# Kernel tuning notes

Hardware: AMD Instinct MI355X
Metric: run time of the kernel (lower is better)

The kernel has to match this reference:

```python
import jax, jax.numpy as jnp
import numpy as np

B = 512        # batch
TW = 45        # raw wav token length
C = 512        # n_embd
H = 8          # heads
L = 8          # decoder layers
V = 1000       # wav vocab
NLAB = 5       # label vocab
HID = 2048     # 4*C mlp hidden
OH = 768       # output head hidden
WIN, TRAIN = 30, 44
LN_EPS = 1e-5


def _build_mask(t):
    # triangular (strict upper) + sliding-window lower band, tiled 3x3 over segments
    m = np.triu(np.ones((TRAIN, TRAIN), dtype=bool), 1)
    for i in range(WIN, TRAIN):
        m[i, : i - WIN + 1] = True
    m = m[:t, :t]
    return jnp.asarray(np.tile(m, (3, 3)))  # [3t, 3t], True = masked


def setup_inputs() -> dict:
    key = jax.random.key(0)
    ks = iter(jax.random.split(key, 64))

    def rn(shape, s=0.02):
        return jax.random.normal(next(ks), shape, jnp.float32) * s

    inp = {
        'label': jax.random.randint(next(ks), (B, 1), 0, NLAB),
        'wav1': jax.random.randint(next(ks), (B, TW), 0, V),
        'wav2': jax.random.randint(next(ks), (B, TW), 0, V),
        # embeddings
        'emb_label': rn((NLAB, C), 1.0),
        'emb_w1': rn((V, C), 1.0),
        'emb_w2': rn((V, C), 1.0),
        # per-layer stacked params (leading dim L) for lax.scan
        'ln1_g': jnp.ones((L, 3, C), jnp.float32),
        'ln1_b': jnp.zeros((L, 3, C), jnp.float32),
        'ln2_g': jnp.ones((L, 3, C), jnp.float32),
        'ln2_b': jnp.zeros((L, 3, C), jnp.float32),
        'Wq': rn((L, C, C)), 'bq': jnp.zeros((L, C), jnp.float32),
        'Wk': rn((L, C, C)), 'bk': jnp.zeros((L, C), jnp.float32),
        'Wv': rn((L, C, C)), 'bv': jnp.zeros((L, C), jnp.float32),
        'Wp': rn((L, C, C)), 'bp': jnp.zeros((L, C), jnp.float32),
        'W1': rn((L, C, HID)), 'b1': jnp.zeros((L, HID), jnp.float32),
        'W2': rn((L, HID, C)), 'b2': jnp.zeros((L, C), jnp.float32),
        # output heads
        'o1W1': rn((C, OH)), 'o1b1': jnp.zeros((OH,), jnp.float32),
        'o1W2': rn((OH, V)), 'o1b2': jnp.zeros((V,), jnp.float32),
        'o2W1': rn((C, OH)), 'o2b1': jnp.zeros((OH,), jnp.float32),
        'o2W2': rn((OH, V)), 'o2b2': jnp.zeros((V,), jnp.float32),
    }
    return inp


def _forward(label, wav1, wav2, emb_label, emb_w1, emb_w2,
             ln1_g, ln1_b, ln2_g, ln2_b, Wq, bq, Wk, bk, Wv, bv, Wp, bp,
             W1, b1, W2, b2, o1W1, o1b1, o1W2, o1b2, o2W1, o2b1, o2W2, o2b2):
    wav1_src, wav1_tgt = wav1[:, :-1], wav1[:, 1:]
    wav2_src, wav2_tgt = wav2[:, :-1], wav2[:, 1:]
    b, t = wav1_src.shape
    label_rep = jnp.broadcast_to(label, (b, t))

    feat = jnp.concatenate([emb_label[label_rep], emb_w1[wav1_src], emb_w2[wav2_src]], axis=1)  # [B,3t,C]
    mask = _build_mask(t)  # [3t,3t] bool
    hd = C // H

    def ln3(x, g, be):
        # three separate LayerNorms over the 3 equal segments
        xr = x.reshape(b, 3, t, C)
        mu = xr.mean(-1, keepdims=True)
        var = xr.var(-1, keepdims=True)
        xn = (xr - mu) * jax.lax.rsqrt(var + LN_EPS)
        return (xn * g[None, :, None, :] + be[None, :, None, :]).reshape(b, 3 * t, C)

    def layer(x, p):
        g1, be1, g2, be2, wq, bq_, wk, bk_, wv, bv_, wp, bp_, w1, b1_, w2, b2_ = p
        h = ln3(x, g1, be1)
        q = (h @ wq + bq_).reshape(b, 3 * t, H, hd).transpose(0, 2, 1, 3)
        k = (h @ wk + bk_).reshape(b, 3 * t, H, hd).transpose(0, 2, 1, 3)
        v = (h @ wv + bv_).reshape(b, 3 * t, H, hd).transpose(0, 2, 1, 3)
        att = jnp.einsum('bhqd,bhkd->bhqk', q, k) * (1.0 / np.sqrt(hd))
        att = jnp.where(mask[None, None], -jnp.inf, att)
        att = jax.nn.softmax(att, axis=-1)
        y = jnp.einsum('bhqk,bhkd->bhqd', att, v).transpose(0, 2, 1, 3).reshape(b, 3 * t, C)
        x = x + (y @ wp + bp_)
        h2 = ln3(x, g2, be2)
        m = jax.nn.gelu(h2 @ w1 + b1_, approximate=False) @ w2 + b2_
        return x + m, None

    params = (ln1_g, ln1_b, ln2_g, ln2_b, Wq, bq, Wk, bk, Wv, bv, Wp, bp, W1, b1, W2, b2)
    x, _ = jax.lax.scan(layer, feat, params)

    wav1_pred = (x[:, t:2 * t] @ o1W1 + o1b1) @ o1W2 + o1b2  # [B,t,V]
    wav2_pred = (x[:, 2 * t:] @ o2W1 + o2b1) @ o2W2 + o2b2

    def ce(logits, tgt):
        lp = jax.nn.log_softmax(logits.reshape(-1, V).astype(jnp.float32), axis=-1)
        return -jnp.mean(jnp.take_along_axis(lp, tgt.reshape(-1, 1), axis=1))

    return ce(wav1_pred, wav1_tgt) + ce(wav2_pred, wav2_tgt)


def reference(label, wav1, wav2, emb_label, emb_w1, emb_w2,
              ln1_g, ln1_b, ln2_g, ln2_b, Wq, bq, Wk, bk, Wv, bv, Wp, bp,
              W1, b1, W2, b2, o1W1, o1b1, o1W2, o1b2, o2W1, o2b1, o2W2, o2b2):
    return _forward(label, wav1, wav2, emb_label, emb_w1, emb_w2,
                    ln1_g, ln1_b, ln2_g, ln2_b, Wq, bq, Wk, bk, Wv, bv, Wp, bp,
                    W1, b1, W2, b2, o1W1, o1b1, o1W2, o1b2, o2W1, o2b1, o2W2, o2b2)
```

## Files before the change

kernel.cpp:

```cpp
#include <hip/hip_runtime.h>

typedef __attribute__((ext_vector_type(4))) float f32x4;
typedef __attribute__((ext_vector_type(8))) __bf16 bf16x8;
typedef __attribute__((ext_vector_type(4))) __bf16 bf16x4;
typedef __attribute__((ext_vector_type(2))) __bf16 bf16x2;
typedef __attribute__((ext_vector_type(8))) unsigned short u16x8;

#define NB 512
#define TT 44
#define S3 132
#define CC 512
#define NH 8
#define NL 8
#define NV 1000
#define VP 1024
#define HID 2048
#define OH 768
#define WINW 30
#define QKVN 1536

#define HROWS (NB*TT)

#define WT_OFF   0ull
#define WC1T_OFF 50331648ull
#define WC2T_OFF 51380224ull
#define BC1_OFF  52428800ull
#define BC2_OFF  52432896ull
#define BQKV_OFF 52436992ull
#define LOSS_OFF 52486144ull
#define FIXED_SZ 52666368ull
#define PER_CHB  811008ull

#define LAYER_WELEMS 3145728ull

__device__ inline bf16x8 zero8() { u16x8 z = (u16x8)0; return *(bf16x8*)&z; }

#define STAGE(bufi, ktile) do { \
  _Pragma("unroll") \
  for (int i_ = 0; i_ < 2; ++i_) { \
    int off_ = wid * 2048 + i_ * 1024; \
    int myoff_ = off_ + lane * 16; \
    int row_ = myoff_ >> 6; \
    int colb_ = (myoff_ & 63) ^ ((row_ & 3) << 4); \
    const char* sa_ = (const char*)(A + (arow + row_) * (size_t)KDIM + ((size_t)(ktile) << 5)) + colb_; \
    const char* sb_ = (const char*)(Bt + (brow + row_) * (size_t)KDIM + ((size_t)(ktile) << 5)) + colb_; \
    __builtin_amdgcn_global_load_lds((const __attribute__((address_space(1))) void*)sa_, \
        (__attribute__((address_space(3))) void*)((char*)&As[bufi][0] + off_), 16, 0, 0); \
    __builtin_amdgcn_global_load_lds((const __attribute__((address_space(1))) void*)sb_, \
        (__attribute__((address_space(3))) void*)((char*)&Bs[bufi][0] + off_), 16, 0, 0); \
  } \
} while (0)

#define PHASE(CURB, KTV, MORE) do { \
  bf16x8 af_[4], bfv_[4]; \
  _Pragma("unroll") \
  for (int mi_ = 0; mi_ < 4; ++mi_) \
    af_[mi_] = *(const bf16x8*)&As[CURB][(wr * 64 + mi_ * 16 + l15) * 32 + ((lk ^ swz) * 8)]; \
  _Pragma("unroll") \
  for (int ni_ = 0; ni_ < 4; ++ni_) \
    bfv_[ni_] = *(const bf16x8*)&Bs[CURB][(wc * 64 + ni_ * 16 + l15) * 32 + ((lk ^ swz) * 8)]; \
  if (MORE) STAGE(((CURB) + 2) % 3, (KTV) + 2); \
  _Pragma("unroll") \
  for (int mi_ = 0; mi_ < 4; ++mi_) \
    _Pragma("unroll") \
    for (int ni_ = 0; ni_ < 4; ++ni_) \
      acc[mi_][ni_] = __builtin_amdgcn_mfma_f32_16x16x32_bf16(af_[mi_], bfv_[ni_], acc[mi_][ni_], 0, 0, 0); \
  if (MORE) { asm volatile("s_waitcnt vmcnt(4)\n\ts_barrier" ::: "memory"); } \
  else      { asm volatile("s_waitcnt vmcnt(0)\n\ts_barrier" ::: "memory"); } \
} while (0)

template<int KDIM, int EPI, typename OutT, typename ResT>
__global__ __launch_bounds__(256) void gemm_bt(
    const __bf16* __restrict__ A, const __bf16* __restrict__ Bt,
    const float* __restrict__ bias, const ResT* __restrict__ resid,
    OutT* __restrict__ C, int M, int N)
{
    __shared__ __bf16 As[3][128 * 32];
    __shared__ __bf16 Bs[3][128 * 32];
    const int tid = threadIdx.x, lane = tid & 63, wid = tid >> 6;
    const int l15 = lane & 15, lk = lane >> 4;
    const int wr = wid >> 1, wc = wid & 1;
    const int swz = l15 & 3;

    const int nwg = gridDim.x * gridDim.y;
    const int orig = blockIdx.y * gridDim.x + blockIdx.x;
    const int qq = nwg >> 3, rr = nwg & 7;
    const int xcd = orig & 7, loc = orig >> 3;
    const int wg = (xcd < rr ? xcd * (qq + 1) : rr * (qq + 1) + (xcd - rr) * qq) + loc;
    const int bn = wg % gridDim.x, bm = wg / gridDim.x;

    f32x4 acc[4][4];
#pragma unroll
    for (int i = 0; i < 4; ++i)
#pragma unroll
        for (int j = 0; j < 4; ++j) acc[i][j] = (f32x4)0.f;

    const size_t arow = (size_t)bm * 128;
    const size_t brow = (size_t)bn * 128;
    constexpr int KT = KDIM >> 5;
    constexpr int M3 = (KT - 2) / 3;

    STAGE(0, 0);
    STAGE(1, 1);
    asm volatile("s_waitcnt vmcnt(4)\n\ts_barrier" ::: "memory");

    for (int t3 = 0; t3 < M3; ++t3) {
        const int kt = t3 * 3;
        PHASE(0, kt, true);
        PHASE(1, kt + 1, true);
        PHASE(2, kt + 2, true);
    }
#pragma unroll
    for (int p = 3 * M3; p < KT; ++p) {
        const int pb = p % 3;
        if (pb == 0)      { if (p <= KT - 3) PHASE(0, p, true); else PHASE(0, p, false); }
        else if (pb == 1) { if (p <= KT - 3) PHASE(1, p, true); else PHASE(1, p, false); }
        else              { if (p <= KT - 3) PHASE(2, p, true); else PHASE(2, p, false); }
    }

#pragma unroll
    for (int mi = 0; mi < 4; ++mi) {
#pragma unroll
        for (int ni = 0; ni < 4; ++ni) {
            int n = bn * 128 + wc * 64 + ni * 16 + l15;
            float bv = (EPI & 1) ? bias[n] : 0.f;
#pragma unroll
            for (int r = 0; r < 4; ++r) {
                int m = bm * 128 + wr * 64 + mi * 16 + lk * 4 + r;
                float v = acc[mi][ni][r] + bv;
                if (EPI & 2) v += (float)resid[(size_t)m * N + n];
                if (EPI & 4) v = v / (1.f + __expf(-1.702f * v));
                C[(size_t)m * N + n] = (OutT)v;
            }
        }
    }
}

#define KLS 68
#define VTS 164
__global__ __launch_bounds__(256) void attn_k(const __bf16* __restrict__ QKV,
                                              __bf16* __restrict__ Y)
{
    __shared__ __bf16 Kl[144 * KLS];
    __shared__ __bf16 Ql[144 * KLS];
    __shared__ __bf16 Vt[64 * VTS];
    __shared__ __bf16 Pl[4][16 * VTS];
    const int tid = threadIdx.x, lane = tid & 63, wid = tid >> 6;
    const int l15 = lane & 15, lk = lane >> 4;
    const int bh = blockIdx.x;
    const int b = bh >> 3, h = bh & 7;
    const size_t base = ((size_t)b * S3) * QKVN + h * 64;
    const size_t ybase = ((size_t)b * S3) * CC + h * 64;

    for (int i = tid; i < S3 * 8; i += 256) {
        int s = i >> 3, c = (i & 7) * 8;
        bf16x8 qv = *(const bf16x8*)(QKV + base + (size_t)s * QKVN + c);
        bf16x8 kv = *(const bf16x8*)(QKV + base + (size_t)s * QKVN + 512 + c);
        *(bf16x8*)&Ql[s * KLS + c] = qv;
        *(bf16x8*)&Kl[s * KLS + c] = kv;
    }
    for (int i = tid; i < (S3 / 2) * 8; i += 256) {
        int s2 = i >> 3, d0 = (i & 7) * 8;
        int s = s2 * 2;
        bf16x8 v0 = *(const bf16x8*)(QKV + base + (size_t)s * QKVN + 1024 + d0);
        bf16x8 v1 = *(const bf16x8*)(QKV + base + (size_t)(s + 1) * QKVN + 1024 + d0);
#pragma unroll
        for (int j = 0; j < 8; ++j) {
            bf16x2 pr; pr[0] = v0[j]; pr[1] = v1[j];
            *(bf16x2*)&Vt[(d0 + j) * VTS + s] = pr;
        }
    }
    for (int i = tid; i < 64 * 32; i += 256) {
        int d = i >> 5, s = 132 + (i & 31);
        Vt[d * VTS + s] = (__bf16)0.f;
    }
    for (int i = lane; i < 16 * 20; i += 64) {
        int r = i / 20, c2 = 144 + (i % 20);
        Pl[wid][r * VTS + c2] = (__bf16)0.f;
    }
    __syncthreads();

    for (int qb = wid; qb < 9; qb += 4) {
        int sq = qb * 16 + l15;
        int sqe = sq < S3 ? sq : (S3 - 1);
        bf16x8 qf0 = *(const bf16x8*)&Ql[(qb * 16 + l15) * KLS + 0 * 32 + lk * 8];
        bf16x8 qf1 = *(const bf16x8*)&Ql[(qb * 16 + l15) * KLS + 1 * 32 + lk * 8];
        f32x4 st[9];
#pragma unroll
        for (int kt = 0; kt < 9; ++kt) {
            f32x4 a = (f32x4)0.f;
            bf16x8 kf0 = *(const bf16x8*)&Kl[(kt * 16 + l15) * KLS + 0 * 32 + lk * 8];
            bf16x8 kf1 = *(const bf16x8*)&Kl[(kt * 16 + l15) * KLS + 1 * 32 + lk * 8];
            a = __builtin_amdgcn_mfma_f32_16x16x32_bf16(kf0, qf0, a, 0, 0, 0);
            a = __builtin_amdgcn_mfma_f32_16x16x32_bf16(kf1, qf1, a, 0, 0, 0);
            st[kt] = a;
        }
        int qm = sqe % TT;
        float mx = -1e30f;
#pragma unroll
        for (int kt = 0; kt < 9; ++kt)
#pragma unroll
            for (int r = 0; r < 4; ++r) {
                int sk = kt * 16 + lk * 4 + r;
                float sv = st[kt][r] * 0.125f;
                int kk = sk % TT;
                bool msk = (sk >= S3) || (kk > qm) || (qm >= WINW && kk <= qm - WINW);
                sv = msk ? -INFINITY : sv;
                st[kt][r] = sv;
                mx = fmaxf(mx, sv);
            }
        mx = fmaxf(mx, __shfl_xor(mx, 16));
        mx = fmaxf(mx, __shfl_xor(mx, 32));
        float sum = 0.f;
#pragma unroll
        for (int kt = 0; kt < 9; ++kt)
#pragma unroll
            for (int r = 0; r < 4; ++r) {
                float p = __expf(st[kt][r] - mx);
                st[kt][r] = p;
                sum += p;
            }
        sum += __shfl_xor(sum, 16);
        sum += __shfl_xor(sum, 32);
        float inv = 1.f / sum;
#pragma unroll
        for (int kt = 0; kt < 9; ++kt) {
            bf16x4 pk;
#pragma unroll
            for (int r = 0; r < 4; ++r) pk[r] = (__bf16)(st[kt][r] * inv);
            *(bf16x4*)&Pl[wid][l15 * VTS + kt * 16 + lk * 4] = pk;
        }
#pragma unroll
        for (int dt = 0; dt < 4; ++dt) {
            f32x4 o = (f32x4)0.f;
#pragma unroll
            for (int ks = 0; ks < 5; ++ks) {
                bf16x8 pa = *(const bf16x8*)&Pl[wid][l15 * VTS + ks * 32 + lk * 8];
                bf16x8 vb = *(const bf16x8*)&Vt[(dt * 16 + l15) * VTS + ks * 32 + lk * 8];
                o = __builtin_amdgcn_mfma_f32_16x16x32_bf16(pa, vb, o, 0, 0, 0);
            }
            int d = dt * 16 + l15;
#pragma unroll
            for (int r = 0; r < 4; ++r) {
                int sqr = qb * 16 + lk * 4 + r;
                if (sqr < S3) Y[ybase + (size_t)sqr * CC + d] = (__bf16)o[r];
            }
        }
    }
}

__global__ __launch_bounds__(256) void ln3_k(const __bf16* __restrict__ X,
                                             const float* __restrict__ g,
                                             const float* __restrict__ be,
                                             __bf16* __restrict__ Hb)
{
    int row = blockIdx.x * 4 + (threadIdx.x >> 6);
    int lane = threadIdx.x & 63;
    int seg = (row % S3) / TT;
    bf16x8 xv = *(const bf16x8*)(X + (size_t)row * CC + lane * 8);
    float vv[8];
    float s = 0.f, ss = 0.f;
#pragma unroll
    for (int j = 0; j < 8; ++j) { vv[j] = (float)xv[j]; s += vv[j]; ss += vv[j] * vv[j]; }
#pragma unroll
    for (int o = 32; o; o >>= 1) { s += __shfl_xor(s, o); ss += __shfl_xor(ss, o); }
    float mu = s * (1.f / CC);
    float var = ss * (1.f / CC) - mu * mu;
    float rs = rsqrtf(var + 1e-5f);
    const float* gp = g + seg * CC + lane * 8;
    const float* bp = be + seg * CC + lane * 8;
    __bf16* op = Hb + (size_t)row * CC + lane * 8;
#pragma unroll
    for (int j = 0; j < 8; ++j) op[j] = (__bf16)((vv[j] - mu) * rs * gp[j] + bp[j]);
}

__global__ __launch_bounds__(128) void embed_k(const int* __restrict__ label,
                                               const int* __restrict__ wav1,
                                               const int* __restrict__ wav2,
                                               const float* __restrict__ el,
                                               const float* __restrict__ e1,
                                               const float* __restrict__ e2,
                                               __bf16* __restrict__ X, int b0)
{
    int row = blockIdx.x;
    int b = b0 + row / S3, p = row % S3;
    int seg = p / TT, pos = p % TT;
    int idx; const float* src;
    if (seg == 0) { idx = label[b]; src = el; }
    else if (seg == 1) { idx = wav1[b * 45 + pos]; src = e1; }
    else { idx = wav2[b * 45 + pos]; src = e2; }
    float4 v = *((const float4*)(src + (size_t)idx * CC) + threadIdx.x);
    __bf16* dst = X + (size_t)row * CC + threadIdx.x * 4;
    dst[0] = (__bf16)v.x; dst[1] = (__bf16)v.y; dst[2] = (__bf16)v.z; dst[3] = (__bf16)v.w;
}

__global__ void transpose_cast(const float* __restrict__ in, __bf16* __restrict__ out,
                               int R, int Cin, int Np, long long inStride, long long outStride)
{
    __shared__ float t[32][33];
    in += (size_t)blockIdx.z * inStride;
    out += (size_t)blockIdx.z * outStride;
    int r0 = blockIdx.x * 32, c0 = blockIdx.y * 32;
    int tx = threadIdx.x, ty = threadIdx.y;
#pragma unroll
    for (int k2 = 0; k2 < 4; ++k2) {
        int r = r0 + ty + k2 * 8, c = c0 + tx;
        t[ty + k2 * 8][tx] = (r < R && c < Cin) ? in[(size_t)r * Cin + c] : 0.f;
    }
    __syncthreads();
#pragma unroll
    for (int k2 = 0; k2 < 4; ++k2) {
        int c = c0 + ty + k2 * 8, r = r0 + tx;
        if (c < Np && r < R) out[(size_t)c * R + r] = (__bf16)t[tx][ty + k2 * 8];
    }
}

__global__ void cast_k(const float* __restrict__ in, __bf16* __restrict__ out, int n)
{
    int i = blockIdx.x * 256 + threadIdx.x;
    if (i < n) out[i] = (__bf16)in[i];
}

__global__ void build_bqkv(const float* __restrict__ bq, const float* __restrict__ bk,
                           const float* __restrict__ bv, float* __restrict__ out)
{
    int i = blockIdx.x * 256 + threadIdx.x;
    if (i >= NL * QKVN) return;
    int l = i / QKVN, c = i % QKVN;
    float v = (c < 512) ? bq[l * 512 + c] : (c < 1024 ? bk[l * 512 + c - 512] : bv[l * 512 + c - 1024]);
    out[i] = v;
}

__global__ __launch_bounds__(128) void gather_cast(const __bf16* __restrict__ X,
                                                   __bf16* __restrict__ out, int segoff)
{
    int row = blockIdx.x;
    int b = row / TT, s2 = row % TT;
    const uint2* src = (const uint2*)(X + ((size_t)b * S3 + segoff + s2) * CC) + threadIdx.x;
    uint2* dst = (uint2*)(out + (size_t)row * CC) + threadIdx.x;
    *dst = *src;
}

__global__ __launch_bounds__(256) void combo_bias(const float* __restrict__ b1,
                                                  const float* __restrict__ W2,
                                                  const float* __restrict__ b2,
                                                  float* __restrict__ out)
{
    int v = blockIdx.x;
    if (v >= VP) return;
    float s = 0.f;
    if (v < NV) {
        for (int o = threadIdx.x; o < OH; o += 256) s += b1[o] * W2[o * NV + v];
    }
#pragma unroll
    for (int o = 32; o; o >>= 1) s += __shfl_xor(s, o);
    __shared__ float w4[4];
    if ((threadIdx.x & 63) == 0) w4[threadIdx.x >> 6] = s;
    __syncthreads();
    if (threadIdx.x == 0) out[v] = (v < NV ? b2[v] : 0.f) + w4[0] + w4[1] + w4[2] + w4[3];
}

__global__ __launch_bounds__(256) void ce_k(const float* __restrict__ logits,
                                            const int* __restrict__ wav,
                                            float* __restrict__ loss)
{
    int row = blockIdx.x * 4 + (threadIdx.x >> 6);
    int lane = threadIdx.x & 63;
    const float* lg = logits + (size_t)row * VP;
    int b = row / TT, s2 = row % TT;
    int tgt = wav[b * 45 + s2 + 1];
    float m = -1e30f;
    for (int i = lane; i < NV; i += 64) m = fmaxf(m, lg[i]);
#pragma unroll
    for (int o = 32; o; o >>= 1) m = fmaxf(m, __shfl_xor(m, o));
    float sum = 0.f;
    for (int i = lane; i < NV; i += 64) sum += __expf(lg[i] - m);
#pragma unroll
    for (int o = 32; o; o >>= 1) sum += __shfl_xor(sum, o);
    if (lane == 0) loss[row] = m + logf(sum) - lg[tgt];
}

__global__ __launch_bounds__(256) void ce_sum(const float* __restrict__ loss, float* __restrict__ out)
{
    float s = 0.f;
    for (int i = threadIdx.x; i < 2 * HROWS; i += 256) s += loss[i];
#pragma unroll
    for (int o = 32; o; o >>= 1) s += __shfl_xor(s, o);
    __shared__ float w4[4];
    if ((threadIdx.x & 63) == 0) w4[threadIdx.x >> 6] = s;
    __syncthreads();
    if (threadIdx.x == 0) out[0] = (w4[0] + w4[1] + w4[2] + w4[3]) * (1.f / HROWS);
}

extern "C" void kernel_launch(void* const* d_in, const int* in_sizes, int n_in,
                              void* d_out, int out_size, void* d_ws, size_t ws_size,
                              hipStream_t stream)
{
    int chb;
    if      (ws_size >= FIXED_SZ + 512ull * PER_CHB) chb = 512;
    else if (ws_size >= FIXED_SZ + 256ull * PER_CHB) chb = 256;
    else if (ws_size >= FIXED_SZ + 128ull * PER_CHB) chb = 128;
    else return;
    const int nch = NB / chb;
    const int crows = chb * S3;
    const int chr = chb * TT;

    const int*   label = (const int*)d_in[0];
    const int*   wav1  = (const int*)d_in[1];
    const int*   wav2  = (const int*)d_in[2];
    const float* el    = (const float*)d_in[3];
    const float* e1    = (const float*)d_in[4];
    const float* e2    = (const float*)d_in[5];
    const float* ln1g  = (const float*)d_in[6];
    const float* ln1b  = (const float*)d_in[7];
    const float* ln2g  = (const float*)d_in[8];
    const float* ln2b  = (const float*)d_in[9];
    const float* Wq    = (const float*)d_in[10];
    const float* bq    = (const float*)d_in[11];
    const float* Wk    = (const float*)d_in[12];
    const float* bk    = (const float*)d_in[13];
    const float* Wv    = (const float*)d_in[14];
    const float* bv    = (const float*)d_in[15];
    const float* Wp    = (const float*)d_in[16];
    const float* bp    = (const float*)d_in[17];
    const float* W1    = (const float*)d_in[18];
    const float* b1    = (const float*)d_in[19];
    const float* W2    = (const float*)d_in[20];
    const float* b2    = (const float*)d_in[21];
    const float* o1W1  = (const float*)d_in[22];
    const float* o1b1  = (const float*)d_in[23];
    const float* o1W2  = (const float*)d_in[24];
    const float* o1b2  = (const float*)d_in[25];
    const float* o2W1  = (const float*)d_in[26];
    const float* o2b1  = (const float*)d_in[27];
    const float* o2W2  = (const float*)d_in[28];
    const float* o2b2  = (const float*)d_in[29];

    char* ws = (char*)d_ws;
    __bf16* WT    = (__bf16*)(ws + WT_OFF);
    __bf16* Wc1T  = (__bf16*)(ws + WC1T_OFF);
    __bf16* Wc2T  = (__bf16*)(ws + WC2T_OFF);
    float*  bc1   = (float*)(ws + BC1_OFF);
    float*  bc2   = (float*)(ws + BC2_OFF);
    float*  bqkv  = (float*)(ws + BQKV_OFF);
    float*  lossb = (float*)(ws + LOSS_OFF);
    __bf16* X     = (__bf16*)(ws + FIXED_SZ);
    __bf16* Hb    = (__bf16*)(ws + FIXED_SZ + (size_t)chb * 135168ull);
    char*   AR    = ws + FIXED_SZ + (size_t)chb * 270336ull;
    __bf16* o1W2T = (__bf16*)(AR + 0);
    __bf16* o2W2T = (__bf16*)(AR + 1572864);
    __bf16* o1W1b = (__bf16*)(AR + 3145728);
    __bf16* o2W1b = (__bf16*)(AR + 3932160);
    __bf16* qkvb   = (__bf16*)AR;
    __bf16* yb_    = Hb;
    __bf16* hidden = (__bf16*)AR;
    float*  logits = (float*)AR;
    __bf16* Xseg   = Hb;
    float*  outF   = (float*)d_out;

    dim3 tb(32, 8);
    transpose_cast<<<dim3(16, 16, NL), tb, 0, stream>>>(Wq, WT + 0,       CC, CC, CC, (long long)CC * CC, (long long)LAYER_WELEMS);
    transpose_cast<<<dim3(16, 16, NL), tb, 0, stream>>>(Wk, WT + 262144,  CC, CC, CC, (long long)CC * CC, (long long)LAYER_WELEMS);
    transpose_cast<<<dim3(16, 16, NL), tb, 0, stream>>>(Wv, WT + 524288,  CC, CC, CC, (long long)CC * CC, (long long)LAYER_WELEMS);
    transpose_cast<<<dim3(16, 16, NL), tb, 0, stream>>>(Wp, WT + 786432,  CC, CC, CC, (long long)CC * CC, (long long)LAYER_WELEMS);
    transpose_cast<<<dim3(16, 64, NL), tb, 0, stream>>>(W1, WT + 1048576, CC, HID, HID, (long long)CC * HID, (long long)LAYER_WELEMS);
    transpose_cast<<<dim3(64, 16, NL), tb, 0, stream>>>(W2, WT + 2097152, HID, CC, CC, (long long)HID * CC, (long long)LAYER_WELEMS);
    transpose_cast<<<dim3(24, 32, 1), tb, 0, stream>>>(o1W2, o1W2T, OH, NV, VP, 0, 0);
    transpose_cast<<<dim3(24, 32, 1), tb, 0, stream>>>(o2W2, o2W2T, OH, NV, VP, 0, 0);
    cast_k<<<(CC * OH + 255) / 256, 256, 0, stream>>>(o1W1, o1W1b, CC * OH);
    cast_k<<<(CC * OH + 255) / 256, 256, 0, stream>>>(o2W1, o2W1b, CC * OH);
    gemm_bt<OH, 0, __bf16, float><<<dim3(4, 8), 256, 0, stream>>>(o1W2T, o1W1b, nullptr, nullptr, Wc1T, VP, CC);
    gemm_bt<OH, 0, __bf16, float><<<dim3(4, 8), 256, 0, stream>>>(o2W2T, o2W1b, nullptr, nullptr, Wc2T, VP, CC);
    combo_bias<<<VP, 256, 0, stream>>>(o1b1, o1W2, o1b2, bc1);
    combo_bias<<<VP, 256, 0, stream>>>(o2b1, o2W2, o2b2, bc2);
    build_bqkv<<<(NL * QKVN + 255) / 256, 256, 0, stream>>>(bq, bk, bv, bqkv);

    for (int c = 0; c < nch; ++c) {
        int b0 = c * chb;
        embed_k<<<crows, 128, 0, stream>>>(label, wav1, wav2, el, e1, e2, X, b0);

        for (int l = 0; l < NL; ++l) {
            const __bf16* WqkvT = WT + (size_t)l * LAYER_WELEMS;
            const __bf16* WpT   = WT + (size_t)l * LAYER_WELEMS + 786432;
            const __bf16* W1T   = WT + (size_t)l * LAYER_WELEMS + 1048576;
            const __bf16* W2T   = WT + (size_t)l * LAYER_WELEMS + 2097152;

            ln3_k<<<crows / 4, 256, 0, stream>>>(X, ln1g + l * 3 * CC, ln1b + l * 3 * CC, Hb);
            gemm_bt<CC, 1, __bf16, float><<<dim3(QKVN / 128, crows / 128), 256, 0, stream>>>(Hb, WqkvT, bqkv + l * QKVN, nullptr, qkvb, crows, QKVN);
            attn_k<<<chb * NH, 256, 0, stream>>>(qkvb, yb_);
            gemm_bt<CC, 3, __bf16, __bf16><<<dim3(4, crows / 128), 256, 0, stream>>>(yb_, WpT, bp + l * CC, X, X, crows, CC);
            ln3_k<<<crows / 4, 256, 0, stream>>>(X, ln2g + l * 3 * CC, ln2b + l * 3 * CC, Hb);
            gemm_bt<CC, 5, __bf16, float><<<dim3(16, crows / 128), 256, 0, stream>>>(Hb, W1T, b1 + l * HID, nullptr, hidden, crows, HID);
            gemm_bt<HID, 3, __bf16, __bf16><<<dim3(4, crows / 128), 256, 0, stream>>>(hidden, W2T, b2 + l * CC, X, X, crows, CC);
        }

        gather_cast<<<chr, 128, 0, stream>>>(X, Xseg, TT);
        gemm_bt<CC, 1, float, float><<<dim3(VP / 128, chr / 128), 256, 0, stream>>>(Xseg, Wc1T, bc1, nullptr, logits, chr, VP);
        ce_k<<<chr / 4, 256, 0, stream>>>(logits, wav1 + b0 * 45, lossb + c * chr);
        gather_cast<<<chr, 128, 0, stream>>>(X, Xseg, 2 * TT);
        gemm_bt<CC, 1, float, float><<<dim3(VP / 128, chr / 128), 256, 0, stream>>>(Xseg, Wc2T, bc2, nullptr, logits, chr, VP);
        ce_k<<<chr / 4, 256, 0, stream>>>(logits, wav2 + b0 * 45, lossb + HROWS + c * chr);
    }

    ce_sum<<<1, 256, 0, stream>>>(lossb, outF);
}
```

Before: 7.333 ms.

## Skip fully masked attention tiles, fuse segment gather into head GEMM, bf16 logits

Precomputes a per-lane validity mask in attention and skips QK MFMAs, masking and exp work for 16-key tiles that are fully masked across the wavefront. It removes the gather_cast kernel by adding an EPI flag that remaps A rows to the wav segments inside the GEMM loads. It also writes the output-head logits as bf16 and reads them as bf16 pairs in the cross-entropy kernel, halving logits traffic. Storing logits in bf16 may reduce loss precision, and the divergent tile skipping adds branching.

```diff
diff --git a/kernel.cpp b/kernel.cpp
--- a/kernel.cpp
+++ b/kernel.cpp
@@ -35,6 +35,8 @@
 
 __device__ inline bf16x8 zero8() { u16x8 z = (u16x8)0; return *(bf16x8*)&z; }
 
+#define AROW(hr_) ((EPI & 8) ? (size_t)(((unsigned)(hr_) / 44u) * 132u + (unsigned)segoff + ((unsigned)(hr_) % 44u)) : (size_t)(hr_))
+
 #define STAGE(bufi, ktile) do { \
   _Pragma("unroll") \
   for (int i_ = 0; i_ < 2; ++i_) { \
@@ -42,7 +44,7 @@
     int myoff_ = off_ + lane * 16; \
     int row_ = myoff_ >> 6; \
     int colb_ = (myoff_ & 63) ^ ((row_ & 3) << 4); \
-    const char* sa_ = (const char*)(A + (arow + row_) * (size_t)KDIM + ((size_t)(ktile) << 5)) + colb_; \
+    const char* sa_ = (const char*)(A + AROW(arow + row_) * (size_t)KDIM + ((size_t)(ktile) << 5)) + colb_; \
     const char* sb_ = (const char*)(Bt + (brow + row_) * (size_t)KDIM + ((size_t)(ktile) << 5)) + colb_; \
     __builtin_amdgcn_global_load_lds((const __attribute__((address_space(1))) void*)sa_, \
         (__attribute__((address_space(3))) void*)((char*)&As[bufi][0] + off_), 16, 0, 0); \
@@ -73,7 +75,7 @@
 __global__ __launch_bounds__(256) void gemm_bt(
     const __bf16* __restrict__ A, const __bf16* __restrict__ Bt,
     const float* __restrict__ bias, const ResT* __restrict__ resid,
-    OutT* __restrict__ C, int M, int N)
+    OutT* __restrict__ C, int M, int N, int segoff)
 {
     __shared__ __bf16 As[3][128 * 32];
     __shared__ __bf16 Bs[3][128 * 32];
@@ -183,43 +185,65 @@
     for (int qb = wid; qb < 9; qb += 4) {
         int sq = qb * 16 + l15;
         int sqe = sq < S3 ? sq : (S3 - 1);
+        int qm = sqe % TT;
+        unsigned long long lmask = 0ull;
+#pragma unroll
+        for (int kt = 0; kt < 9; ++kt)
+#pragma unroll
+            for (int r = 0; r < 4; ++r) {
+                int sk = kt * 16 + lk * 4 + r;
+                int kk = sk % TT;
+                bool ok = (sk < S3) && (kk <= qm) && (qm < WINW || kk > qm - WINW);
+                if (ok) lmask |= 1ull << (kt * 4 + r);
+            }
+        unsigned needmask = 0;
+#pragma unroll
+        for (int kt = 0; kt < 9; ++kt)
+            if (__any((int)((lmask >> (kt * 4)) & 15ull))) needmask |= 1u << kt;
+
         bf16x8 qf0 = *(const bf16x8*)&Ql[(qb * 16 + l15) * KLS + 0 * 32 + lk * 8];
         bf16x8 qf1 = *(const bf16x8*)&Ql[(qb * 16 + l15) * KLS + 1 * 32 + lk * 8];
         f32x4 st[9];
 #pragma unroll
         for (int kt = 0; kt < 9; ++kt) {
-            f32x4 a = (f32x4)0.f;
-            bf16x8 kf0 = *(const bf16x8*)&Kl[(kt * 16 + l15) * KLS + 0 * 32 + lk * 8];
-            bf16x8 kf1 = *(const bf16x8*)&Kl[(kt * 16 + l15) * KLS + 1 * 32 + lk * 8];
-            a = __builtin_amdgcn_mfma_f32_16x16x32_bf16(kf0, qf0, a, 0, 0, 0);
-            a = __builtin_amdgcn_mfma_f32_16x16x32_bf16(kf1, qf1, a, 0, 0, 0);
-            st[kt] = a;
-        }
-        int qm = sqe % TT;
+            if (needmask & (1u << kt)) {
+                f32x4 a = (f32x4)0.f;
+                bf16x8 kf0 = *(const bf16x8*)&Kl[(kt * 16 + l15) * KLS + 0 * 32 + lk * 8];
+                bf16x8 kf1 = *(const bf16x8*)&Kl[(kt * 16 + l15) * KLS + 1 * 32 + lk * 8];
+                a = __builtin_amdgcn_mfma_f32_16x16x32_bf16(kf0, qf0, a, 0, 0, 0);
+                a = __builtin_amdgcn_mfma_f32_16x16x32_bf16(kf1, qf1, a, 0, 0, 0);
+                st[kt] = a;
+            }
+        }
         float mx = -1e30f;
 #pragma unroll
-        for (int kt = 0; kt < 9; ++kt)
-#pragma unroll
-            for (int r = 0; r < 4; ++r) {
-                int sk = kt * 16 + lk * 4 + r;
-                float sv = st[kt][r] * 0.125f;
-                int kk = sk % TT;
-                bool msk = (sk >= S3) || (kk > qm) || (qm >= WINW && kk <= qm - WINW);
-                sv = msk ? -INFINITY : sv;
-                st[kt][r] = sv;
-                mx = fmaxf(mx, sv);
-            }
+        for (int kt = 0; kt < 9; ++kt) {
+            if (needmask & (1u << kt)) {
+#pragma unroll
+                for (int r = 0; r < 4; ++r) {
+                    bool ok = (lmask >> (kt * 4 + r)) & 1ull;
+                    float sv = ok ? st[kt][r] * 0.125f : -INFINITY;
+                    st[kt][r] = sv;
+                    mx = fmaxf(mx, sv);
+                }
+            }
+        }
         mx = fmaxf(mx, __shfl_xor(mx, 16));
         mx = fmaxf(mx, __shfl_xor(mx, 32));
         float sum = 0.f;
 #pragma unroll
-        for (int kt = 0; kt < 9; ++kt)
-#pragma unroll
-            for (int r = 0; r < 4; ++r) {
-                float p = __expf(st[kt][r] - mx);
-                st[kt][r] = p;
-                sum += p;
-            }
+        for (int kt = 0; kt < 9; ++kt) {
+            if (needmask & (1u << kt)) {
+#pragma unroll
+                for (int r = 0; r < 4; ++r) {
+                    float p = __expf(st[kt][r] - mx);
+                    st[kt][r] = p;
+                    sum += p;
+                }
+            } else {
+                st[kt] = (f32x4)0.f;
+            }
+        }
         sum += __shfl_xor(sum, 16);
         sum += __shfl_xor(sum, 32);
         float inv = 1.f / sum;
@@ -331,16 +355,6 @@
     out[i] = v;
 }
 
-__global__ __launch_bounds__(128) void gather_cast(const __bf16* __restrict__ X,
-                                                   __bf16* __restrict__ out, int segoff)
-{
-    int row = blockIdx.x;
-    int b = row / TT, s2 = row % TT;
-    const uint2* src = (const uint2*)(X + ((size_t)b * S3 + segoff + s2) * CC) + threadIdx.x;
-    uint2* dst = (uint2*)(out + (size_t)row * CC) + threadIdx.x;
-    *dst = *src;
-}
-
 __global__ __launch_bounds__(256) void combo_bias(const float* __restrict__ b1,
                                                   const float* __restrict__ W2,
                                                   const float* __restrict__ b2,
@@ -360,24 +374,30 @@
     if (threadIdx.x == 0) out[v] = (v < NV ? b2[v] : 0.f) + w4[0] + w4[1] + w4[2] + w4[3];
 }
 
-__global__ __launch_bounds__(256) void ce_k(const float* __restrict__ logits,
+__global__ __launch_bounds__(256) void ce_k(const __bf16* __restrict__ logits,
                                             const int* __restrict__ wav,
                                             float* __restrict__ loss)
 {
     int row = blockIdx.x * 4 + (threadIdx.x >> 6);
     int lane = threadIdx.x & 63;
-    const float* lg = logits + (size_t)row * VP;
+    const __bf16* lg = logits + (size_t)row * VP;
     int b = row / TT, s2 = row % TT;
     int tgt = wav[b * 45 + s2 + 1];
     float m = -1e30f;
-    for (int i = lane; i < NV; i += 64) m = fmaxf(m, lg[i]);
+    for (int i2 = lane; i2 < NV / 2; i2 += 64) {
+        bf16x2 pr = *(const bf16x2*)(lg + 2 * i2);
+        m = fmaxf(m, fmaxf((float)pr[0], (float)pr[1]));
+    }
 #pragma unroll
     for (int o = 32; o; o >>= 1) m = fmaxf(m, __shfl_xor(m, o));
     float sum = 0.f;
-    for (int i = lane; i < NV; i += 64) sum += __expf(lg[i] - m);
+    for (int i2 = lane; i2 < NV / 2; i2 += 64) {
+        bf16x2 pr = *(const bf16x2*)(lg + 2 * i2);
+        sum += __expf((float)pr[0] - m) + __expf((float)pr[1] - m);
+    }
 #pragma unroll
     for (int o = 32; o; o >>= 1) sum += __shfl_xor(sum, o);
-    if (lane == 0) loss[row] = m + logf(sum) - lg[tgt];
+    if (lane == 0) loss[row] = m + logf(sum) - (float)lg[tgt];
 }
 
 __global__ __launch_bounds__(256) void ce_sum(const float* __restrict__ loss, float* __restrict__ out)
@@ -451,12 +471,11 @@
     __bf16* o2W2T = (__bf16*)(AR + 1572864);
     __bf16* o1W1b = (__bf16*)(AR + 3145728);
     __bf16* o2W1b = (__bf16*)(AR + 3932160);
-    __bf16* qkvb   = (__bf16*)AR;
-    __bf16* yb_    = Hb;
-    __bf16* hidden = (__bf16*)AR;
-    float*  logits = (float*)AR;
-    __bf16* Xseg   = Hb;
-    float*  outF   = (float*)d_out;
+    __bf16* qkvb    = (__bf16*)AR;
+    __bf16* yb_     = Hb;
+    __bf16* hidden  = (__bf16*)AR;
+    __bf16* logitsB = (__bf16*)AR;
+    float*  outF    = (float*)d_out;
 
     dim3 tb(32, 8);
     transpose_cast<<<dim3(16, 16, NL), tb, 0, stream>>>(Wq, WT + 0,       CC, CC, CC, (long long)CC * CC, (long long)LAYER_WELEMS);
@@ -469,8 +488,8 @@
     transpose_cast<<<dim3(24, 32, 1), tb, 0, stream>>>(o2W2, o2W2T, OH, NV, VP, 0, 0);
     cast_k<<<(CC * OH + 255) / 256, 256, 0, stream>>>(o1W1, o1W1b, CC * OH);
     cast_k<<<(CC * OH + 255) / 256, 256, 0, stream>>>(o2W1, o2W1b, CC * OH);
-    gemm_bt<OH, 0, __bf16, float><<<dim3(4, 8), 256, 0, stream>>>(o1W2T, o1W1b, nullptr, nullptr, Wc1T, VP, CC);
-    gemm_bt<OH, 0, __bf16, float><<<dim3(4, 8), 256, 0, stream>>>(o2W2T, o2W1b, nullptr, nullptr, Wc2T, VP, CC);
+    gemm_bt<OH, 0, __bf16, float><<<dim3(4, 8), 256, 0, stream>>>(o1W2T, o1W1b, nullptr, nullptr, Wc1T, VP, CC, 0);
+    gemm_bt<OH, 0, __bf16, float><<<dim3(4, 8), 256, 0, stream>>>(o2W2T, o2W1b, nullptr, nullptr, Wc2T, VP, CC, 0);
     combo_bias<<<VP, 256, 0, stream>>>(o1b1, o1W2, o1b2, bc1);
     combo_bias<<<VP, 256, 0, stream>>>(o2b1, o2W2, o2b2, bc2);
     build_bqkv<<<(NL * QKVN + 255) / 256, 256, 0, stream>>>(bq, bk, bv, bqkv);
@@ -486,20 +505,18 @@
             const __bf16* W2T   = WT + (size_t)l * LAYER_WELEMS + 2097152;
 
             ln3_k<<<crows / 4, 256, 0, stream>>>(X, ln1g + l * 3 * CC, ln1b + l * 3 * CC, Hb);
-            gemm_bt<CC, 1, __bf16, float><<<dim3(QKVN / 128, crows / 128), 256, 0, stream>>>(Hb, WqkvT, bqkv + l * QKVN, nullptr, qkvb, crows, QKVN);
+            gemm_bt<CC, 1, __bf16, float><<<dim3(QKVN / 128, crows / 128), 256, 0, stream>>>(Hb, WqkvT, bqkv + l * QKVN, nullptr, qkvb, crows, QKVN, 0);
             attn_k<<<chb * NH, 256, 0, stream>>>(qkvb, yb_);
-            gemm_bt<CC, 3, __bf16, __bf16><<<dim3(4, crows / 128), 256, 0, stream>>>(yb_, WpT, bp + l * CC, X, X, crows, CC);
+            gemm_bt<CC, 3, __bf16, __bf16><<<dim3(4, crows / 128), 256, 0, stream>>>(yb_, WpT, bp + l * CC, X, X, crows, CC, 0);
             ln3_k<<<crows / 4, 256, 0, stream>>>(X, ln2g + l * 3 * CC, ln2b + l * 3 * CC, Hb);
-            gemm_bt<CC, 5, __bf16, float><<<dim3(16, crows / 128), 256, 0, stream>>>(Hb, W1T, b1 + l * HID, nullptr, hidden, crows, HID);
-            gemm_bt<HID, 3, __bf16, __bf16><<<dim3(4, crows / 128), 256, 0, stream>>>(hidden, W2T, b2 + l * CC, X, X, crows, CC);
-        }
-
-        gather_cast<<<chr, 128, 0, stream>>>(X, Xseg, TT);
-        gemm_bt<CC, 1, float, float><<<dim3(VP / 128, chr / 128), 256, 0, stream>>>(Xseg, Wc1T, bc1, nullptr, logits, chr, VP);
-        ce_k<<<chr / 4, 256, 0, stream>>>(logits, wav1 + b0 * 45, lossb + c * chr);
-        gather_cast<<<chr, 128, 0, stream>>>(X, Xseg, 2 * TT);
-        gemm_bt<CC, 1, float, float><<<dim3(VP / 128, chr / 128), 256, 0, stream>>>(Xseg, Wc2T, bc2, nullptr, logits, chr, VP);
-        ce_k<<<chr / 4, 256, 0, stream>>>(logits, wav2 + b0 * 45, lossb + HROWS + c * chr);
+            gemm_bt<CC, 5, __bf16, float><<<dim3(16, crows / 128), 256, 0, stream>>>(Hb, W1T, b1 + l * HID, nullptr, hidden, crows, HID, 0);
+            gemm_bt<HID, 3, __bf16, __bf16><<<dim3(4, crows / 128), 256, 0, stream>>>(hidden, W2T, b2 + l * CC, X, X, crows, CC, 0);
+        }
+
+        gemm_bt<CC, 9, __bf16, float><<<dim3(VP / 128, chr / 128), 256, 0, stream>>>(X, Wc1T, bc1, nullptr, logitsB, chr, VP, TT);
+        ce_k<<<chr / 4, 256, 0, stream>>>(logitsB, wav1 + b0 * 45, lossb + c * chr);
+        gemm_bt<CC, 9, __bf16, float><<<dim3(VP / 128, chr / 128), 256, 0, stream>>>(X, Wc2T, bc2, nullptr, logitsB, chr, VP, 2 * TT);
+        ce_k<<<chr / 4, 256, 0, stream>>>(logitsB, wav2 + b0 * 45, lossb + HROWS + c * chr);
     }
 
     ce_sum<<<1, 256, 0, stream>>>(lossb, outF);
```

Result: slower. 7.878 ms (+7.4%).
